# Kernel tuning notes

Measured on AMD Instinct MI355X. Metric: run time of the kernel, lower is better.

The kernel has to match this reference:

```python
import jax, jax.numpy as jnp
import numpy as np

L, B, ENC, ATTN, HID = 2048, 32, 1024, 1024, 1024


def setup_inputs() -> dict:
    key = jax.random.key(0)
    k1, k2, k3, k4, k5 = jax.random.split(key, 5)
    return {
        "enc_outputs": jax.random.normal(k1, (L, B, ENC), dtype=jnp.float32),
        "mask": jnp.zeros((L, B), dtype=jnp.float32),
        "hidden_state": jax.random.normal(k2, (B, HID), dtype=jnp.float32),
        "W_enc": jax.random.normal(k3, (ENC, ATTN), dtype=jnp.float32) * (2.0 / (ENC + ATTN)) ** 0.5,
        "b_attn": jnp.zeros((ATTN,), dtype=jnp.float32),
        "W_hidden": jax.random.normal(k4, (HID, ATTN), dtype=jnp.float32) * (2.0 / (HID + ATTN)) ** 0.5,
        "v": jax.random.normal(k5, (ATTN,), dtype=jnp.float32) * 0.1,
    }


def reference(enc_outputs, mask, hidden_state, W_enc, b_attn, W_hidden, v):
    # keys: [l, b, attn]  (map_enc=False so values = enc_outputs)
    keys = jnp.einsum('lbe,ea->lba', enc_outputs, W_enc) + b_attn
    values = enc_outputs
    # query projection: [b, attn], broadcast over l
    q = hidden_state @ W_hidden
    # additive Bahdanau score -> [l, b]
    alignment = jnp.einsum('lba,a->lb', jnp.tanh(keys + q[None, :, :]), v)
    # masked softmax over time (dim 0)
    alignment = jax.nn.softmax(mask + alignment, axis=0)
    # weighted value sum -> context [b, enc]
    context = jnp.einsum('lb,lbe->be', alignment, values)
    return (context, alignment)
```

## Files before the change

### kernel.cpp

```cpp
#include <hip/hip_runtime.h>
#include <stdint.h>

#define L_DIM 2048
#define B_DIM 32
#define ENC_DIM 1024
#define M_DIM (L_DIM * B_DIM)

typedef __attribute__((ext_vector_type(4))) float f32x4;
typedef __attribute__((ext_vector_type(4))) unsigned int uint4v;
typedef __attribute__((ext_vector_type(8))) short short8;
typedef __attribute__((ext_vector_type(4))) short short4v;
typedef __attribute__((ext_vector_type(4))) __bf16 bf16x4;

static __device__ __forceinline__ float fast_tanh(float x) {
  float cx = fminf(fmaxf(x, -15.f), 15.f);
  float e = __expf(2.f * cx);
  return (e - 1.f) * __frcp_rn(e + 1.f);
}

static __device__ __forceinline__ float bf2f(unsigned short u) {
  return __builtin_bit_cast(float, (unsigned int)u << 16);
}

static __device__ __forceinline__ void load_lds16(const void* g, void* l) {
  __builtin_amdgcn_global_load_lds((const __attribute__((address_space(1))) void*)g,
                                   (__attribute__((address_space(3))) void*)l, 16, 0, 0);
}

__global__ __launch_bounds__(256) void k_enc_bf16(const float* __restrict__ enc,
                                                  unsigned short* __restrict__ encB) {
  const int t = blockIdx.x * 256 + threadIdx.x;
#pragma unroll
  for (int it = 0; it < 16; ++it) {
    size_t i = ((size_t)t + (size_t)it * 524288) << 3;
    f32x4 a = *reinterpret_cast<const f32x4*>(enc + i);
    f32x4 b = *reinterpret_cast<const f32x4*>(enc + i + 4);
    bf16x4 pa = {(__bf16)a.x, (__bf16)a.y, (__bf16)a.z, (__bf16)a.w};
    bf16x4 pb = {(__bf16)b.x, (__bf16)b.y, (__bf16)b.z, (__bf16)b.w};
    union { bf16x4 v; unsigned int u[2]; } ua, ub;
    ua.v = pa; ub.v = pb;
    uint4v o;
    o.x = ua.u[0]; o.y = ua.u[1]; o.z = ub.u[0]; o.w = ub.u[1];
    *reinterpret_cast<uint4v*>(encB + i) = o;
  }
}

__global__ __launch_bounds__(256) void k_wt(const float* __restrict__ W,
                                            unsigned short* __restrict__ WT) {
  __shared__ float tile[64][65];
  const int t = threadIdx.x;
  const int k0 = (blockIdx.x & 15) << 6, n0 = (blockIdx.x >> 4) << 6;
#pragma unroll
  for (int i = 0; i < 16; ++i) {
    int idx = t + (i << 8);
    tile[idx >> 6][idx & 63] = W[(size_t)(k0 + (idx >> 6)) * 1024 + n0 + (idx & 63)];
  }
  __syncthreads();
#pragma unroll
  for (int i = 0; i < 16; ++i) {
    int idx = t + (i << 8);
    int r = idx >> 6, c = idx & 63;
    WT[(size_t)(n0 + r) * 1024 + k0 + c] =
        __builtin_bit_cast(unsigned short, (__bf16)tile[c][r]);
  }
}

__global__ __launch_bounds__(128) void k_qpart(const float* __restrict__ hidden,
                                               const float* __restrict__ Wh,
                                               float* __restrict__ pq) {
  const int ablk = blockIdx.x & 7, hblk = blockIdx.x >> 3;
  const int a = (ablk << 7) + threadIdx.x;
  float acc[32];
#pragma unroll
  for (int b = 0; b < 32; ++b) acc[b] = 0.f;
  const int h0 = hblk << 7;
  for (int h = h0; h < h0 + 128; ++h) {
    float wv = Wh[(size_t)h * 1024 + a];
#pragma unroll
    for (int b = 0; b < 32; ++b) acc[b] = fmaf(hidden[(b << 10) + h], wv, acc[b]);
  }
#pragma unroll
  for (int b = 0; b < 32; ++b) pq[((size_t)hblk << 15) + (b << 10) + a] = acc[b];
}

__global__ __launch_bounds__(256) void k_qred(const float* __restrict__ pq,
                                              const float* __restrict__ ba,
                                              float* __restrict__ q) {
  int i = blockIdx.x * 256 + threadIdx.x;
  float s = ba[i & 1023];
#pragma unroll
  for (int j = 0; j < 8; ++j) s += pq[((size_t)j << 15) + i];
  q[i] = s;
}


__global__ __launch_bounds__(256, 4) void k_logits_bf(const unsigned short* __restrict__ encB,
                                                      const unsigned short* __restrict__ WT,
                                                      const float* __restrict__ qv,
                                                      const float* __restrict__ v,
                                                      float* __restrict__ pl) {
  __shared__ __align__(16) unsigned short As[128 * 64];
  __shared__ __align__(16) unsigned short Bs[128 * 64];
  __shared__ float red[2][128];

  const int tid = threadIdx.x;
  const int xcd = blockIdx.x & 7, slot = blockIdx.x >> 3;
  const int nblk = slot & 7;
  const int mblk = xcd + ((slot >> 3) << 3);
  const int row0 = mblk << 7;
  const int n0 = nblk << 7;

  const int w = tid >> 6, lane = tid & 63;
  const int wr = w >> 1, wc = w & 1;
  const int g = lane >> 4, rr = lane & 15;

  float vreg[4];
#pragma unroll
  for (int nf = 0; nf < 4; ++nf) vreg[nf] = v[n0 + wc * 64 + nf * 16 + rr];

  f32x4 acc[4][4];
#pragma unroll
  for (int mf = 0; mf < 4; ++mf)
#pragma unroll
    for (int nf = 0; nf < 4; ++nf)
#pragma unroll
      for (int rg = 0; rg < 4; ++rg) {
        int b = ((mf & 1) << 4) + (g << 2) + rg;
        acc[mf][nf][rg] = qv[((size_t)b << 10) + n0 + wc * 64 + nf * 16 + rr];
      }

  const int srow = lane >> 3, sjj = lane & 7;

  for (int kt = 0; kt < 16; ++kt) {
    const int k0 = kt << 6;
    __syncthreads();
#pragma unroll
    for (int c = 0; c < 4; ++c) {
      int r = w * 32 + c * 8 + srow;
      int blk = sjj ^ (r & 7);
      const char* bsrc = (const char*)WT + (((size_t)(n0 + r) << 10) + k0) * 2 + (blk << 4);
      load_lds16(bsrc, (void*)&Bs[(w * 32 + c * 8) * 64]);
      const char* asrc = (const char*)encB + (((size_t)(row0 + r) << 10) + k0) * 2 + (blk << 4);
      load_lds16(asrc, (void*)&As[(w * 32 + c * 8) * 64]);
    }
    __syncthreads();
#pragma unroll
    for (int kk = 0; kk < 2; ++kk) {
      short8 af[4], bfr[4];
#pragma unroll
      for (int mf = 0; mf < 4; ++mf) {
        int r = wr * 64 + mf * 16 + rr;
        int blk = (kk * 4 + g) ^ (r & 7);
        af[mf] = *reinterpret_cast<const short8*>(&As[r * 64 + (blk << 3)]);
      }
#pragma unroll
      for (int nf = 0; nf < 4; ++nf) {
        int r = wc * 64 + nf * 16 + rr;
        int blk = (kk * 4 + g) ^ (r & 7);
        bfr[nf] = *reinterpret_cast<const short8*>(&Bs[r * 64 + (blk << 3)]);
      }
#pragma unroll
      for (int mf = 0; mf < 4; ++mf)
#pragma unroll
        for (int nf = 0; nf < 4; ++nf)
          acc[mf][nf] = __builtin_amdgcn_mfma_f32_16x16x32_bf16(af[mf], bfr[nf], acc[mf][nf], 0, 0, 0);
    }
  }

#pragma unroll
  for (int mf = 0; mf < 4; ++mf) {
#pragma unroll
    for (int rg = 0; rg < 4; ++rg) {
      int lrow = wr * 64 + mf * 16 + g * 4 + rg;
      float s = 0.f;
#pragma unroll
      for (int nf = 0; nf < 4; ++nf) s += fast_tanh(acc[mf][nf][rg]) * vreg[nf];
      s += __shfl_xor(s, 1);
      s += __shfl_xor(s, 2);
      s += __shfl_xor(s, 4);
      s += __shfl_xor(s, 8);
      if (rr == 0) red[wc][lrow] = s;
    }
  }
  __syncthreads();
  if (tid < 128) {
    int row = row0 + tid;
    pl[((size_t)nblk << 16) + ((size_t)(row & 31) << 11) + (row >> 5)] =
        red[0][tid] + red[1][tid];
  }
}

__global__ __launch_bounds__(256, 3) void k_logits_cvt(const float* __restrict__ enc,
                                                       const unsigned short* __restrict__ WT,
                                                       const float* __restrict__ qv,
                                                       const float* __restrict__ v,
                                                       float* __restrict__ pl) {
  __shared__ __align__(16) unsigned short As[128 * 64];
  __shared__ __align__(16) unsigned short Bs[128 * 64];
  __shared__ float red[2][128];

  const int tid = threadIdx.x;
  const int xcd = blockIdx.x & 7, slot = blockIdx.x >> 3;
  const int nblk = slot & 7;
  const int mblk = xcd + ((slot >> 3) << 3);
  const int row0 = mblk << 7;
  const int n0 = nblk << 7;

  const int w = tid >> 6, lane = tid & 63;
  const int wr = w >> 1, wc = w & 1;
  const int g = lane >> 4, rr = lane & 15;

  float vreg[4];
#pragma unroll
  for (int nf = 0; nf < 4; ++nf) vreg[nf] = v[n0 + wc * 64 + nf * 16 + rr];

  f32x4 acc[4][4];
#pragma unroll
  for (int mf = 0; mf < 4; ++mf)
#pragma unroll
    for (int nf = 0; nf < 4; ++nf)
#pragma unroll
      for (int rg = 0; rg < 4; ++rg) {
        int b = ((mf & 1) << 4) + (g << 2) + rg;
        acc[mf][nf][rg] = qv[((size_t)b << 10) + n0 + wc * 64 + nf * 16 + rr];
      }

  const int ar = tid >> 4;
  const int ac4 = tid & 15;
  const int ablk = ((ac4 >> 1) ^ (ar & 7));
  const int brow = lane >> 3, bjj = lane & 7;

  for (int kt = 0; kt < 16; ++kt) {
    const int k0 = kt << 6;
    __syncthreads();
#pragma unroll
    for (int c = 0; c < 4; ++c) {
      int nrow = w * 32 + c * 8 + brow;
      int blk = bjj ^ (brow & 7);
      const char* src = (const char*)WT + (((size_t)(n0 + nrow) << 10) + k0) * 2 + (blk << 4);
      load_lds16(src, (void*)&Bs[(w * 32 + c * 8) * 64]);
    }
#pragma unroll
    for (int i = 0; i < 8; ++i) {
      int r = ar + (i << 4);
      f32x4 a4 = *reinterpret_cast<const f32x4*>(enc + (((size_t)(row0 + r)) << 10) + k0 + (ac4 << 2));
      bf16x4 pk = {(__bf16)a4.x, (__bf16)a4.y, (__bf16)a4.z, (__bf16)a4.w};
      *reinterpret_cast<bf16x4*>(&As[r * 64 + (ablk << 3) + ((ac4 & 1) << 2)]) = pk;
    }
    __syncthreads();
#pragma unroll
    for (int kk = 0; kk < 2; ++kk) {
      short8 af[4], bfr[4];
#pragma unroll
      for (int mf = 0; mf < 4; ++mf) {
        int r = wr * 64 + mf * 16 + rr;
        int blk = (kk * 4 + g) ^ (r & 7);
        af[mf] = *reinterpret_cast<const short8*>(&As[r * 64 + (blk << 3)]);
      }
#pragma unroll
      for (int nf = 0; nf < 4; ++nf) {
        int r = wc * 64 + nf * 16 + rr;
        int blk = (kk * 4 + g) ^ (r & 7);
        bfr[nf] = *reinterpret_cast<const short8*>(&Bs[r * 64 + (blk << 3)]);
      }
#pragma unroll
      for (int mf = 0; mf < 4; ++mf)
#pragma unroll
        for (int nf = 0; nf < 4; ++nf)
          acc[mf][nf] = __builtin_amdgcn_mfma_f32_16x16x32_bf16(af[mf], bfr[nf], acc[mf][nf], 0, 0, 0);
    }
  }

#pragma unroll
  for (int mf = 0; mf < 4; ++mf) {
#pragma unroll
    for (int rg = 0; rg < 4; ++rg) {
      int lrow = wr * 64 + mf * 16 + g * 4 + rg;
      float s = 0.f;
#pragma unroll
      for (int nf = 0; nf < 4; ++nf) s += fast_tanh(acc[mf][nf][rg]) * vreg[nf];
      s += __shfl_xor(s, 1);
      s += __shfl_xor(s, 2);
      s += __shfl_xor(s, 4);
      s += __shfl_xor(s, 8);
      if (rr == 0) red[wc][lrow] = s;
    }
  }
  __syncthreads();
  if (tid < 128) {
    int row = row0 + tid;
    pl[((size_t)nblk << 16) + ((size_t)(row & 31) << 11) + (row >> 5)] =
        red[0][tid] + red[1][tid];
  }
}

__global__ __launch_bounds__(256) void k_softmax(const float* __restrict__ pl,
                                                 const float* __restrict__ mask,
                                                 float* __restrict__ al) {
  const int b = blockIdx.x, t = threadIdx.x;
  __shared__ float sr[256];
  float lg[8];
  float mx = -3.4e38f;
#pragma unroll
  for (int i = 0; i < 8; ++i) {
    int l = t + (i << 8);
    float s = mask[(l << 5) + b];
#pragma unroll
    for (int nb = 0; nb < 8; ++nb) s += pl[((size_t)nb << 16) + (b << 11) + l];
    lg[i] = s;
    mx = fmaxf(mx, s);
  }
  sr[t] = mx;
  __syncthreads();
  for (int off = 128; off > 0; off >>= 1) {
    if (t < off) sr[t] = fmaxf(sr[t], sr[t + off]);
    __syncthreads();
  }
  const float M = sr[0];
  __syncthreads();
  float sum = 0.f;
#pragma unroll
  for (int i = 0; i < 8; ++i) {
    lg[i] = __expf(lg[i] - M);
    sum += lg[i];
  }
  sr[t] = sum;
  __syncthreads();
  for (int off = 128; off > 0; off >>= 1) {
    if (t < off) sr[t] += sr[t + off];
    __syncthreads();
  }
  const float inv = 1.f / sr[0];
#pragma unroll
  for (int i = 0; i < 8; ++i) {
    int l = t + (i << 8);
    al[(l << 5) + b] = lg[i] * inv;
  }
}

__global__ __launch_bounds__(256) void k_ctx_bf(const unsigned short* __restrict__ encB,
                                                const float* __restrict__ al,
                                                float* __restrict__ pctx) {
  const int b = blockIdx.x & 31, ch = blockIdx.x >> 5;
  const int t = threadIdx.x;
  __shared__ float wl[64];
  if (t < 64) wl[t] = al[(((ch << 6) + t) << 5) + b];
  __syncthreads();
  f32x4 acc = (f32x4){0.f, 0.f, 0.f, 0.f};
  const unsigned short* base = encB + (((size_t)ch * 2048 + b) << 10) + (t << 2);
#pragma unroll 8
  for (int i = 0; i < 64; ++i) {
    short4v e = *reinterpret_cast<const short4v*>(base + (size_t)i * 32768);
    float w = wl[i];
    acc.x = fmaf(w, bf2f((unsigned short)e[0]), acc.x);
    acc.y = fmaf(w, bf2f((unsigned short)e[1]), acc.y);
    acc.z = fmaf(w, bf2f((unsigned short)e[2]), acc.z);
    acc.w = fmaf(w, bf2f((unsigned short)e[3]), acc.w);
  }
  *reinterpret_cast<f32x4*>(((float*)pctx) + ((size_t)blockIdx.x << 10) + (t << 2)) = acc;
}

__global__ __launch_bounds__(256) void k_ctx(const float* __restrict__ enc,
                                             const float* __restrict__ al,
                                             float* __restrict__ pctx) {
  const int b = blockIdx.x & 31, ch = blockIdx.x >> 5;
  const int t = threadIdx.x;
  __shared__ float wl[64];
  if (t < 64) wl[t] = al[(((ch << 6) + t) << 5) + b];
  __syncthreads();
  f32x4 acc = (f32x4){0.f, 0.f, 0.f, 0.f};
  const float* base = enc + (((size_t)ch * 2048 + b) << 10) + (t << 2);
#pragma unroll 8
  for (int i = 0; i < 64; ++i) {
    f32x4 e = *reinterpret_cast<const f32x4*>(base + (size_t)i * 32768);
    acc += wl[i] * e;
  }
  *reinterpret_cast<f32x4*>(((float*)pctx) + ((size_t)blockIdx.x << 10) + (t << 2)) = acc;
}

__global__ __launch_bounds__(256) void k_ctxred(const float* __restrict__ pctx,
                                                float* __restrict__ out) {
  int i = blockIdx.x * 256 + threadIdx.x;
  int b = i >> 10, e = i & 1023;
  float s = 0.f;
#pragma unroll
  for (int ch = 0; ch < 32; ++ch) s += pctx[(size_t)((ch << 5) + b) * 1024 + e];
  out[i] = s;
}

extern "C" void kernel_launch(void* const* d_in, const int* in_sizes, int n_in,
                              void* d_out, int out_size, void* d_ws, size_t ws_size,
                              hipStream_t stream) {
  const float* enc = (const float*)d_in[0];
  const float* mask = (const float*)d_in[1];
  const float* hidden = (const float*)d_in[2];
  const float* Wenc = (const float*)d_in[3];
  const float* battn = (const float*)d_in[4];
  const float* Whid = (const float*)d_in[5];
  const float* v = (const float*)d_in[6];
  float* out = (float*)d_out;
  char* ws = (char*)d_ws;

  const bool big = ws_size >= (size_t)140 * 1024 * 1024;
  char* base = big ? ws + ((size_t)128 << 20) : ws;
  unsigned short* encB = (unsigned short*)ws;
  unsigned short* WT = (unsigned short*)base;
  float* q = (float*)(base + (2u << 20));
  float* pq = (float*)(base + (2u << 20) + (128u << 10));
  float* pl = (float*)(base + (3u << 20) + (128u << 10));
  float* pctx = (float*)(base + (5u << 20) + (128u << 10));
  float* align_out = out + 32768;

  k_wt<<<256, 256, 0, stream>>>(Wenc, WT);
  k_qpart<<<64, 128, 0, stream>>>(hidden, Whid, pq);
  k_qred<<<128, 256, 0, stream>>>(pq, battn, q);
  if (big) {
    k_enc_bf16<<<2048, 256, 0, stream>>>(enc, encB);
    k_logits_bf<<<4096, 256, 0, stream>>>(encB, WT, q, v, pl);
  } else {
    k_logits_cvt<<<4096, 256, 0, stream>>>(enc, WT, q, v, pl);
  }
  k_softmax<<<32, 256, 0, stream>>>(pl, mask, align_out);
  if (big) {
    k_ctx_bf<<<1024, 256, 0, stream>>>(encB, align_out, pctx);
  } else {
    k_ctx<<<1024, 256, 0, stream>>>(enc, align_out, pctx);
  }
  k_ctxred<<<128, 256, 0, stream>>>(pctx, out);
}
```

Measured before the change: 338.2 us.

## Use 256x256 tiles with double-buffered LDS pipeline in logits GEMM

Replaces the 128x128 single-buffered logits GEMM with a 512-thread kernel that computes 256x256 tiles. It double-buffers the A and B tiles in LDS and issues the next k-slice's global-to-LDS loads while MFMAs run, using barriers and setprio to interleave them. Larger tiles halve the number of N partials, so softmax now sums 4 partials instead of 8, and operand reuse per byte loaded goes up. The cost is higher register and LDS use (64 KB of LDS) and fewer resident blocks per CU.

```diff
diff --git a/kernel.cpp b/kernel.cpp
--- a/kernel.cpp
+++ b/kernel.cpp
@@ -25,6 +25,18 @@
 static __device__ __forceinline__ void load_lds16(const void* g, void* l) {
   __builtin_amdgcn_global_load_lds((const __attribute__((address_space(1))) void*)g,
                                    (__attribute__((address_space(3))) void*)l, 16, 0, 0);
+}
+
+static __device__ __forceinline__ void stage4(const unsigned short* __restrict__ gsrc,
+                                              unsigned short* ldst, int rowbase, int k0s,
+                                              int w, int sr, int sblk) {
+#pragma unroll
+  for (int c = 0; c < 4; ++c) {
+    int rgrp = (w << 2) + c;
+    const char* src = (const char*)gsrc +
+        ((((size_t)(rowbase + (rgrp << 3) + sr) << 10) + k0s + (sblk << 3)) << 1);
+    load_lds16(src, (void*)(ldst + ((size_t)rgrp << 9)));
+  }
 }
 
 __global__ __launch_bounds__(256) void k_enc_bf16(const float* __restrict__ enc,
@@ -93,34 +105,33 @@
   q[i] = s;
 }
 
-
-__global__ __launch_bounds__(256, 4) void k_logits_bf(const unsigned short* __restrict__ encB,
-                                                      const unsigned short* __restrict__ WT,
-                                                      const float* __restrict__ qv,
-                                                      const float* __restrict__ v,
-                                                      float* __restrict__ pl) {
-  __shared__ __align__(16) unsigned short As[128 * 64];
-  __shared__ __align__(16) unsigned short Bs[128 * 64];
-  __shared__ float red[2][128];
+__global__ __launch_bounds__(512, 2) void k_logits8(const unsigned short* __restrict__ encB,
+                                                    const unsigned short* __restrict__ WT,
+                                                    const float* __restrict__ qv,
+                                                    const float* __restrict__ v,
+                                                    float* __restrict__ pl) {
+  __shared__ __align__(16) unsigned short As[2][256 * 64];
+  __shared__ __align__(16) unsigned short Bs[2][256 * 64];
 
   const int tid = threadIdx.x;
   const int xcd = blockIdx.x & 7, slot = blockIdx.x >> 3;
-  const int nblk = slot & 7;
-  const int mblk = xcd + ((slot >> 3) << 3);
-  const int row0 = mblk << 7;
-  const int n0 = nblk << 7;
+  const int nblk = slot & 3;
+  const int mblk = xcd + ((slot >> 2) << 3);
+  const int row0 = mblk << 8;
+  const int n0 = nblk << 8;
 
   const int w = tid >> 6, lane = tid & 63;
-  const int wr = w >> 1, wc = w & 1;
+  const int wr = w >> 2, wc = w & 3;
   const int g = lane >> 4, rr = lane & 15;
+  const int sr = lane >> 3, sb = lane & 7, sblk = sb ^ sr;
 
   float vreg[4];
 #pragma unroll
   for (int nf = 0; nf < 4; ++nf) vreg[nf] = v[n0 + wc * 64 + nf * 16 + rr];
 
-  f32x4 acc[4][4];
-#pragma unroll
-  for (int mf = 0; mf < 4; ++mf)
+  f32x4 acc[8][4];
+#pragma unroll
+  for (int mf = 0; mf < 8; ++mf)
 #pragma unroll
     for (int nf = 0; nf < 4; ++nf)
 #pragma unroll
@@ -129,49 +140,70 @@
         acc[mf][nf][rg] = qv[((size_t)b << 10) + n0 + wc * 64 + nf * 16 + rr];
       }
 
-  const int srow = lane >> 3, sjj = lane & 7;
-
-  for (int kt = 0; kt < 16; ++kt) {
-    const int k0 = kt << 6;
-    __syncthreads();
-#pragma unroll
-    for (int c = 0; c < 4; ++c) {
-      int r = w * 32 + c * 8 + srow;
-      int blk = sjj ^ (r & 7);
-      const char* bsrc = (const char*)WT + (((size_t)(n0 + r) << 10) + k0) * 2 + (blk << 4);
-      load_lds16(bsrc, (void*)&Bs[(w * 32 + c * 8) * 64]);
-      const char* asrc = (const char*)encB + (((size_t)(row0 + r) << 10) + k0) * 2 + (blk << 4);
-      load_lds16(asrc, (void*)&As[(w * 32 + c * 8) * 64]);
-    }
-    __syncthreads();
-#pragma unroll
-    for (int kk = 0; kk < 2; ++kk) {
-      short8 af[4], bfr[4];
-#pragma unroll
-      for (int mf = 0; mf < 4; ++mf) {
-        int r = wr * 64 + mf * 16 + rr;
-        int blk = (kk * 4 + g) ^ (r & 7);
-        af[mf] = *reinterpret_cast<const short8*>(&As[r * 64 + (blk << 3)]);
-      }
-#pragma unroll
-      for (int nf = 0; nf < 4; ++nf) {
-        int r = wc * 64 + nf * 16 + rr;
-        int blk = (kk * 4 + g) ^ (r & 7);
-        bfr[nf] = *reinterpret_cast<const short8*>(&Bs[r * 64 + (blk << 3)]);
-      }
-#pragma unroll
-      for (int mf = 0; mf < 4; ++mf)
+  stage4(encB, &As[0][0], row0, 0, w, sr, sblk);
+  stage4(WT, &Bs[0][0], n0, 0, w, sr, sblk);
+  asm volatile("s_waitcnt vmcnt(0)" ::: "memory");
+  __builtin_amdgcn_sched_barrier(0);
+  __builtin_amdgcn_s_barrier();
+
+#pragma unroll 2
+  for (int t = 0; t < 16; ++t) {
+    const int cur = t & 1;
+    const unsigned short* Ab = &As[cur][0];
+    const unsigned short* Bb = &Bs[cur][0];
+    short8 bfr[4][2];
+
+#pragma unroll
+    for (int q = 0; q < 4; ++q) {
+      if (q == 0) {
 #pragma unroll
         for (int nf = 0; nf < 4; ++nf)
-          acc[mf][nf] = __builtin_amdgcn_mfma_f32_16x16x32_bf16(af[mf], bfr[nf], acc[mf][nf], 0, 0, 0);
-    }
-  }
-
-#pragma unroll
-  for (int mf = 0; mf < 4; ++mf) {
+#pragma unroll
+          for (int kk = 0; kk < 2; ++kk) {
+            int r = wc * 64 + nf * 16 + rr;
+            int blk = (kk * 4 + g) ^ (r & 7);
+            bfr[nf][kk] = *reinterpret_cast<const short8*>(&Bb[r * 64 + (blk << 3)]);
+          }
+      }
+      short8 af[2][2];
+#pragma unroll
+      for (int j = 0; j < 2; ++j)
+#pragma unroll
+        for (int kk = 0; kk < 2; ++kk) {
+          int r = wr * 128 + (2 * q + j) * 16 + rr;
+          int blk = (kk * 4 + g) ^ (r & 7);
+          af[j][kk] = *reinterpret_cast<const short8*>(&Ab[r * 64 + (blk << 3)]);
+        }
+      if (t < 15) {
+        if (q == 0) stage4(encB, &As[cur ^ 1][0], row0, (t + 1) << 6, w, sr, sblk);
+        if (q == 1) stage4(WT, &Bs[cur ^ 1][0], n0, (t + 1) << 6, w, sr, sblk);
+      }
+      __builtin_amdgcn_s_barrier();
+      __builtin_amdgcn_s_setprio(1);
+#pragma unroll
+      for (int j = 0; j < 2; ++j)
+#pragma unroll
+        for (int kk = 0; kk < 2; ++kk)
+#pragma unroll
+          for (int nf = 0; nf < 4; ++nf)
+            acc[2 * q + j][nf] =
+                __builtin_amdgcn_mfma_f32_16x16x32_bf16(af[j][kk], bfr[nf][kk],
+                                                        acc[2 * q + j][nf], 0, 0, 0);
+      __builtin_amdgcn_s_setprio(0);
+      if (q == 3 && t < 15) {
+        asm volatile("s_waitcnt vmcnt(0)" ::: "memory");
+        __builtin_amdgcn_sched_barrier(0);
+      }
+      __builtin_amdgcn_s_barrier();
+    }
+  }
+
+  float* red = reinterpret_cast<float*>(&Bs[0][0]);
+#pragma unroll
+  for (int mf = 0; mf < 8; ++mf) {
 #pragma unroll
     for (int rg = 0; rg < 4; ++rg) {
-      int lrow = wr * 64 + mf * 16 + g * 4 + rg;
+      int lrow = wr * 128 + mf * 16 + g * 4 + rg;
       float s = 0.f;
 #pragma unroll
       for (int nf = 0; nf < 4; ++nf) s += fast_tanh(acc[mf][nf][rg]) * vreg[nf];
@@ -179,14 +211,14 @@
       s += __shfl_xor(s, 2);
       s += __shfl_xor(s, 4);
       s += __shfl_xor(s, 8);
-      if (rr == 0) red[wc][lrow] = s;
-    }
-  }
-  __syncthreads();
-  if (tid < 128) {
+      if (rr == 0) red[wc * 256 + lrow] = s;
+    }
+  }
+  __syncthreads();
+  if (tid < 256) {
     int row = row0 + tid;
     pl[((size_t)nblk << 16) + ((size_t)(row & 31) << 11) + (row >> 5)] =
-        red[0][tid] + red[1][tid];
+        red[tid] + red[256 + tid] + red[512 + tid] + red[768 + tid];
   }
 }
 
@@ -294,6 +326,7 @@
   }
 }
 
+template <int NP>
 __global__ __launch_bounds__(256) void k_softmax(const float* __restrict__ pl,
                                                  const float* __restrict__ mask,
                                                  float* __restrict__ al) {
@@ -306,7 +339,7 @@
     int l = t + (i << 8);
     float s = mask[(l << 5) + b];
 #pragma unroll
-    for (int nb = 0; nb < 8; ++nb) s += pl[((size_t)nb << 16) + (b << 11) + l];
+    for (int nb = 0; nb < NP; ++nb) s += pl[((size_t)nb << 16) + (b << 11) + l];
     lg[i] = s;
     mx = fmaxf(mx, s);
   }
@@ -416,14 +449,12 @@
   k_qred<<<128, 256, 0, stream>>>(pq, battn, q);
   if (big) {
     k_enc_bf16<<<2048, 256, 0, stream>>>(enc, encB);
-    k_logits_bf<<<4096, 256, 0, stream>>>(encB, WT, q, v, pl);
+    k_logits8<<<1024, 512, 0, stream>>>(encB, WT, q, v, pl);
+    k_softmax<4><<<32, 256, 0, stream>>>(pl, mask, align_out);
+    k_ctx_bf<<<1024, 256, 0, stream>>>(encB, align_out, pctx);
   } else {
     k_logits_cvt<<<4096, 256, 0, stream>>>(enc, WT, q, v, pl);
-  }
-  k_softmax<<<32, 256, 0, stream>>>(pl, mask, align_out);
-  if (big) {
-    k_ctx_bf<<<1024, 256, 0, stream>>>(encB, align_out, pctx);
-  } else {
+    k_softmax<8><<<32, 256, 0, stream>>>(pl, mask, align_out);
     k_ctx<<<1024, 256, 0, stream>>>(enc, align_out, pctx);
   }
   k_ctxred<<<128, 256, 0, stream>>>(pctx, out);
```

Result: slower. 369.3 us (+9.2%).
